# Kernel tuning notes

Measured on AMD Instinct MI355X. Metric: run time of the kernel, lower is better.

Reference implementation:

```python
import jax, jax.numpy as jnp
import numpy as np

HEADS = 8  # diffusers default for hidden_size=320 (head_dim=40)


def setup_inputs() -> dict:
    key = jax.random.key(0)
    k0, k1, k2, k3, k4 = jax.random.split(key, 5)
    batches_of_frames, n, S, C = 1, 5, 1024, 320
    to_k_other = 2
    hidden_states = jax.random.normal(k0, (batches_of_frames * n, S, C), jnp.float32)
    Wq = jax.random.normal(k1, (C, C), jnp.float32) * 0.02
    Wk = jax.random.normal(k2, (C, C), jnp.float32) * 0.02
    Wv = jax.random.normal(k3, (C, C), jnp.float32) * 0.02
    Wo = jax.random.normal(k4, (C, C), jnp.float32) * 0.02
    bo = jnp.zeros((C,), jnp.float32)
    # set_config with random_others=False: self id first, then sequential others
    ids = np.array([[i] + [k for k in range(n) if k != i][:to_k_other] for i in range(n)], dtype=np.int64)
    return {"hidden_states": hidden_states, "Wq": Wq, "Wk": Wk, "Wv": Wv,
            "Wo": Wo, "bo": bo, "ids": jnp.asarray(ids)}


def reference(hidden_states, Wq, Wk, Wv, Wo, bo, ids):
    B, S, C = hidden_states.shape
    n, kf = ids.shape            # frames per group, selected frames per query frame
    Bf = B // n                  # batches_of_frames
    H = HEADS
    d = C // H

    q = hidden_states @ Wq                      # [B, S, C]
    k = hidden_states @ Wk
    v = hidden_states @ Wv

    def gather_frames(x):
        x = x.reshape(Bf, n, S, C)              # expand_batch
        x = x[:, ids]                           # [Bf, n, kf, S, C] cross-frame gather
        return x.reshape(Bf * n, kf * S, C)     # collapse_batch

    k = gather_frames(k)                        # [B, kf*S, C]
    v = gather_frames(v)

    q = q.reshape(B, S, H, d).transpose(0, 2, 1, 3)          # [B, H, S, d]
    k = k.reshape(B, kf * S, H, d).transpose(0, 2, 1, 3)     # [B, H, kf*S, d]
    v = v.reshape(B, kf * S, H, d).transpose(0, 2, 1, 3)

    scale = 1.0 / jnp.sqrt(jnp.asarray(d, q.dtype))
    scores = jnp.einsum('bhqd,bhkd->bhqk', q, k) * scale     # [B, H, S, kf*S]
    probs = jax.nn.softmax(scores, axis=-1)
    attn_out = jnp.einsum('bhqk,bhkd->bhqd', probs, v)       # [B, H, S, d]

    out = attn_out.transpose(0, 2, 1, 3).reshape(B, S, C)    # merge heads
    out = out @ Wo + bo                                      # to_out[0]; to_out[1] dropout = identity
    return out + hidden_states                               # residual, rescale_output_factor=1
```

## Files before the change

kernel.cpp:

```cpp
#include <hip/hip_runtime.h>
#include <hip/hip_bf16.h>

#define NB 5
#define NS 1024
#define NC 320
#define NH 8
#define ND 40
#define NKF 3
#define NBS (NB*NS)
#define NL (NKF*NS)
#define HP 48
#define QSTR 384
#define KTILE (32*48)
#define VTILE (64*32)

typedef __attribute__((ext_vector_type(4))) float f32x4;
typedef __attribute__((ext_vector_type(16))) float f32x16;
typedef __attribute__((ext_vector_type(8))) short bf16x8;
typedef __attribute__((ext_vector_type(4))) unsigned u32x4;

#define MFMA16(a,b,c) __builtin_amdgcn_mfma_f32_16x16x32_bf16((a),(b),(c),0,0,0)
#define MFMA32(a,b,c) __builtin_amdgcn_mfma_f32_32x32x16_bf16((a),(b),(c),0,0,0)

#define QSCALE2 0.22811012f

__device__ inline float ex2(float x){
  float r;
  asm("v_exp_f32 %0, %1" : "=v"(r) : "v"(x));
  return r;
}

__device__ inline unsigned short f2bf(float f){
  unsigned int u = __builtin_bit_cast(unsigned int, f);
  u += 0x7fffu + ((u >> 16) & 1u);
  return (unsigned short)(u >> 16);
}

__device__ inline unsigned pkbf(float lo, float hi){
  unsigned r;
  asm("v_cvt_pk_bf16_f32 %0, %1, %2" : "=v"(r) : "v"(lo), "v"(hi));
  return r;
}

__global__ __launch_bounds__(256) void k_conv_hs(const float* __restrict__ hs,
                                                 unsigned short* __restrict__ hsb){
  int i = (blockIdx.x * 256 + threadIdx.x) * 4;
  float4 v = *(const float4*)&hs[i];
  ushort4 o;
  o.x = f2bf(v.x); o.y = f2bf(v.y); o.z = f2bf(v.z); o.w = f2bf(v.w);
  *(ushort4*)&hsb[i] = o;
}

__global__ void k_conv_w(const float* __restrict__ wq, const float* __restrict__ wk,
                         const float* __restrict__ wv, const float* __restrict__ wo,
                         unsigned short* __restrict__ wqT, unsigned short* __restrict__ wkT,
                         unsigned short* __restrict__ wvT, unsigned short* __restrict__ woT){
  int k = blockIdx.x * 16 + threadIdx.x;
  int n = blockIdx.y * 16 + threadIdx.y;
  const float* src; unsigned short* dst; float scl = 1.0f;
  switch (blockIdx.z){
    case 0: src = wq; dst = wqT; scl = QSCALE2; break;
    case 1: src = wk; dst = wkT; break;
    case 2: src = wv; dst = wvT; break;
    default: src = wo; dst = woT; break;
  }
  dst[n*NC + k] = f2bf(src[k*NC + n] * scl);
}

__global__ __launch_bounds__(256) void k_zero_qbpad(unsigned short* __restrict__ qbp){
  int t = blockIdx.x * 256 + threadIdx.x;
  int token = t >> 3, hh = t & 7;
  bf16x8 z = {0,0,0,0,0,0,0,0};
  *(bf16x8*)&qbp[token*QSTR + hh*HP + ND] = z;
}

__global__ __launch_bounds__(256) void k_qkv(const unsigned short* __restrict__ hsb,
    const unsigned short* __restrict__ wqT, const unsigned short* __restrict__ wkT,
    const unsigned short* __restrict__ wvT,
    unsigned short* __restrict__ qb, unsigned short* __restrict__ kb,
    unsigned short* __restrict__ vT){
  int wave = threadIdx.x >> 6, lane = threadIdx.x & 63;
  int lane16 = lane & 15, grp = lane >> 4;
  int m0 = blockIdx.x * 64, n0 = blockIdx.y * 64;
  int mat = blockIdx.z;
  const unsigned short* wT = (mat == 0) ? wqT : ((mat == 1) ? wkT : wvT);
  int arow = m0 + wave * 16 + lane16;
  f32x4 acc[4];
  #pragma unroll
  for (int t = 0; t < 4; t++) acc[t] = (f32x4){0.f,0.f,0.f,0.f};
  #pragma unroll
  for (int k0 = 0; k0 < NC; k0 += 32){
    bf16x8 a = *(const bf16x8*)&hsb[arow*NC + k0 + grp*8];
    #pragma unroll
    for (int t = 0; t < 4; t++){
      bf16x8 b = *(const bf16x8*)&wT[(n0 + t*16 + lane16)*NC + k0 + grp*8];
      acc[t] = MFMA16(a, b, acc[t]);
    }
  }
  int crow = m0 + wave * 16 + grp * 4;
  #pragma unroll
  for (int t = 0; t < 4; t++){
    int cc = n0 + t*16 + lane16;
    int hh = cc / ND, dd = cc - hh*ND;
    #pragma unroll
    for (int r = 0; r < 4; r++){
      unsigned short val = f2bf(acc[t][r]);
      int rr = crow + r;
      int tokblk = rr >> 5, tl = rr & 31;
      if (mat == 0)      qb[rr*QSTR + hh*HP + dd] = val;
      else if (mat == 1) kb[(((size_t)tokblk*NH + hh)*32 + tl)*HP + dd] = val;
      else               vT[(((size_t)tokblk*NH + hh)*64 + dd)*32 + tl] = val;
    }
  }
}

__global__ __launch_bounds__(192, 3) void k_attn(const unsigned short* __restrict__ qb,
    const unsigned short* __restrict__ kb, const unsigned short* __restrict__ vT,
    const int* __restrict__ ids, unsigned short* __restrict__ ao){
  __shared__ float ldsO[NKF][32][64];
  __shared__ float ldsM[NKF][32];
  __shared__ float ldsL[NKF][32];
  __shared__ float ldsCF[NKF][32];
  int w = threadIdx.x >> 6, lane = threadIdx.x & 63;
  int l31 = lane & 31, hi = lane >> 5;
  int b = blockIdx.z;
  int h = blockIdx.x & 7;
  int q0 = (blockIdx.x >> 3) * 32;
  int frame = ids[b*NKF + w];

  bf16x8 qf0, qf1, qf2;
  {
    int qoff = (b*NS + q0 + l31) * QSTR + h*HP + hi*8;
    qf0 = *(const bf16x8*)&qb[qoff];
    qf1 = *(const bf16x8*)&qb[qoff + 16];
    qf2 = *(const bf16x8*)&qb[qoff + 32];
  }

  const unsigned short* kbase = kb + ((size_t)(frame*32)*NH + h)*KTILE + l31*HP + hi*8;
  const unsigned short* vbase = vT + ((size_t)(frame*32)*NH + h)*VTILE + l31*32 + hi*8;

  f32x16 o0, o1;
  #pragma unroll
  for (int r = 0; r < 16; r++){ o0[r] = 0.f; o1[r] = 0.f; }
  const f32x16 z16 = o0;
  float m2 = -1e30f, lsum = 0.f;

  #pragma unroll 2
  for (int kvb = 0; kvb < NS/32; kvb++){
    const unsigned short* kp = kbase + (size_t)kvb * (NH*KTILE);
    const unsigned short* vp = vbase + (size_t)kvb * (NH*VTILE);
    bf16x8 k0 = *(const bf16x8*)(kp);
    bf16x8 k1 = *(const bf16x8*)(kp + 16);
    bf16x8 k2 = *(const bf16x8*)(kp + 32);
    bf16x8 v00 = *(const bf16x8*)(vp);
    bf16x8 v01 = *(const bf16x8*)(vp + 16);
    bf16x8 v10 = *(const bf16x8*)(vp + 32*32);
    bf16x8 v11 = *(const bf16x8*)(vp + 32*32 + 16);

    f32x16 s = MFMA32(k0, qf0, z16);
    s = MFMA32(k1, qf1, s);
    s = MFMA32(k2, qf2, s);

    float t0 = fmaxf(fmaxf(s[0], s[1]), s[2]);
    float t1 = fmaxf(fmaxf(s[3], s[4]), s[5]);
    float t2 = fmaxf(fmaxf(s[6], s[7]), s[8]);
    float t3 = fmaxf(fmaxf(s[9], s[10]), s[11]);
    float t4 = fmaxf(fmaxf(s[12], s[13]), s[14]);
    float pmax = fmaxf(fmaxf(fmaxf(t0, t1), fmaxf(t2, t3)), fmaxf(t4, s[15]));
    pmax = fmaxf(pmax, __shfl_xor(pmax, 32));

    if (!__all(pmax - m2 <= 8.0f)){
      float mnew = fmaxf(m2, pmax);
      float cf = ex2(m2 - mnew);
      lsum *= cf;
      if (lane < 32) ldsCF[w][l31] = cf;
      #pragma unroll
      for (int r = 0; r < 16; r++){
        float c = ldsCF[w][(r&3) + 8*(r>>2) + 4*hi];
        o0[r] *= c; o1[r] *= c;
      }
      m2 = mnew;
    }

    float p[16];
    #pragma unroll
    for (int r = 0; r < 16; r++) p[r] = ex2(s[r] - m2);
    float a0 = (p[0]+p[1]) + (p[2]+p[3]);
    float a1 = (p[4]+p[5]) + (p[6]+p[7]);
    float a2 = (p[8]+p[9]) + (p[10]+p[11]);
    float a3 = (p[12]+p[13]) + (p[14]+p[15]);
    float ts = (a0+a1) + (a2+a3);
    ts += __shfl_xor(ts, 32);
    lsum += ts;

    u32x4 pw0, pw1;
    #pragma unroll
    for (int ks = 0; ks < 2; ks++){
      int qa = 2*ks + hi;
      int qp = 2*ks + 1 - hi;
      unsigned A0 = pkbf(p[4*qa+0], p[4*qa+1]);
      unsigned A1 = pkbf(p[4*qa+2], p[4*qa+3]);
      unsigned B0 = pkbf(p[4*qp+0], p[4*qp+1]);
      unsigned B1 = pkbf(p[4*qp+2], p[4*qp+3]);
      unsigned R0 = (unsigned)__shfl_xor((int)B0, 32);
      unsigned R1 = (unsigned)__shfl_xor((int)B1, 32);
      u32x4 wd;
      if (hi == 0){ wd[0]=A0; wd[1]=A1; wd[2]=R0; wd[3]=R1; }
      else        { wd[0]=R0; wd[1]=R1; wd[2]=A0; wd[3]=A1; }
      if (ks == 0) pw0 = wd; else pw1 = wd;
    }
    bf16x8 pa0 = __builtin_bit_cast(bf16x8, pw0);
    bf16x8 pa1 = __builtin_bit_cast(bf16x8, pw1);

    o0 = MFMA32(pa0, v00, o0);
    o0 = MFMA32(pa1, v01, o0);
    o1 = MFMA32(pa0, v10, o1);
    o1 = MFMA32(pa1, v11, o1);
  }

  #pragma unroll
  for (int r = 0; r < 16; r++){
    int qq = (r&3) + 8*(r>>2) + 4*hi;
    ldsO[w][qq][l31]      = o0[r];
    ldsO[w][qq][32 + l31] = o1[r];
  }
  if (lane < 32){ ldsM[w][l31] = m2; ldsL[w][l31] = lsum; }
  __syncthreads();

  for (int t = threadIdx.x; t < 32*ND; t += 192){
    int qq = t / ND, d = t - (t / ND) * ND;
    float mA = ldsM[0][qq], mB = ldsM[1][qq], mC = ldsM[2][qq];
    float M = fmaxf(fmaxf(mA, mB), mC);
    float eA = ex2(mA - M), eB = ex2(mB - M), eC = ex2(mC - M);
    float L = ldsL[0][qq]*eA + ldsL[1][qq]*eB + ldsL[2][qq]*eC;
    float O = ldsO[0][qq][d]*eA + ldsO[1][qq][d]*eB + ldsO[2][qq][d]*eC;
    ao[(size_t)(b*NS + q0 + qq)*NC + h*ND + d] = f2bf(O / L);
  }
}

__global__ __launch_bounds__(256) void k_out(const unsigned short* __restrict__ ao,
    const unsigned short* __restrict__ woT, const float* __restrict__ bo,
    const float* __restrict__ hs, float* __restrict__ out){
  int wave = threadIdx.x >> 6, lane = threadIdx.x & 63;
  int lane16 = lane & 15, grp = lane >> 4;
  int m0 = blockIdx.x * 64, n0 = blockIdx.y * 64;
  int arow = m0 + wave*16 + lane16;
  f32x4 acc[4];
  #pragma unroll
  for (int t = 0; t < 4; t++) acc[t] = (f32x4){0.f,0.f,0.f,0.f};
  #pragma unroll
  for (int k0 = 0; k0 < NC; k0 += 32){
    bf16x8 a = *(const bf16x8*)&ao[arow*NC + k0 + grp*8];
    #pragma unroll
    for (int t = 0; t < 4; t++){
      bf16x8 b = *(const bf16x8*)&woT[(n0 + t*16 + lane16)*NC + k0 + grp*8];
      acc[t] = MFMA16(a, b, acc[t]);
    }
  }
  int crow = m0 + wave*16 + grp*4;
  #pragma unroll
  for (int t = 0; t < 4; t++){
    int cc = n0 + t*16 + lane16;
    #pragma unroll
    for (int r = 0; r < 4; r++){
      int rr = crow + r;
      out[rr*NC + cc] = acc[t][r] + bo[cc] + hs[rr*NC + cc];
    }
  }
}

extern "C" void kernel_launch(void* const* d_in, const int* in_sizes, int n_in,
                              void* d_out, int out_size, void* d_ws, size_t ws_size,
                              hipStream_t stream){
  const float* hs = (const float*)d_in[0];
  const float* Wq = (const float*)d_in[1];
  const float* Wk = (const float*)d_in[2];
  const float* Wv = (const float*)d_in[3];
  const float* Wo = (const float*)d_in[4];
  const float* bo = (const float*)d_in[5];
  const int*  ids = (const int*)d_in[6];
  float* out = (float*)d_out;

  unsigned short* hsb = (unsigned short*)d_ws;
  unsigned short* wqT = hsb + (size_t)NBS*NC;
  unsigned short* wkT = wqT + (size_t)NC*NC;
  unsigned short* wvT = wkT + (size_t)NC*NC;
  unsigned short* woT = wvT + (size_t)NC*NC;
  unsigned short* qb  = woT + (size_t)NC*NC;
  unsigned short* kb  = qb  + (size_t)NBS*QSTR;
  unsigned short* vT  = kb  + (size_t)(NBS/32)*NH*KTILE;
  unsigned short* ao  = hsb;

  k_conv_hs<<<dim3(NBS*NC/1024), dim3(256), 0, stream>>>(hs, hsb);
  k_conv_w<<<dim3(NC/16, NC/16, 4), dim3(16,16), 0, stream>>>(Wq, Wk, Wv, Wo, wqT, wkT, wvT, woT);
  k_zero_qbpad<<<dim3(NBS*NH/256), dim3(256), 0, stream>>>(qb);
  k_qkv<<<dim3(NBS/64, NC/64, 3), dim3(256), 0, stream>>>(hsb, wqT, wkT, wvT, qb, kb, vT);
  k_attn<<<dim3((NS/32)*NH, 1, NB), dim3(192), 0, stream>>>(qb, kb, vT, ids, ao);
  k_out<<<dim3(NBS/64, NC/64, 1), dim3(256), 0, stream>>>(ao, woT, bo, hs, out);
}
```

Measured before the change: 280.1 us.

## Double-buffer K/V tile loads with inline asm global loads and vmcnt waits

Replaces the compiler-scheduled per-iteration K/V loads in the attention inner loop with a manual two-stage software pipeline. It issues raw global_load_dwordx4 via inline asm for the next tile while computing the current one, and uses s_waitcnt vmcnt(7) plus sched barriers to wait only for the older batch. The aim is to hide global memory latency behind the QK/PV MFMA and softmax work. The cost is more live registers for two buffers, one redundant clamped load on the last iteration, and fragile asm whose vmcnt accounting must match exactly.

```diff
diff --git a/kernel.cpp b/kernel.cpp
--- a/kernel.cpp
+++ b/kernel.cpp
@@ -23,6 +23,9 @@
 #define MFMA32(a,b,c) __builtin_amdgcn_mfma_f32_32x32x16_bf16((a),(b),(c),0,0,0)
 
 #define QSCALE2 0.22811012f
+
+#define GLOAD(dst, ptr) asm volatile("global_load_dwordx4 %0, %1, off" : "=v"(dst) : "v"(ptr))
+#define WAIT7() do{ asm volatile("s_waitcnt vmcnt(7)" ::: "memory"); __builtin_amdgcn_sched_barrier(0); }while(0)
 
 __device__ inline float ex2(float x){
   float r;
@@ -138,6 +141,7 @@
 
   const unsigned short* kbase = kb + ((size_t)(frame*32)*NH + h)*KTILE + l31*HP + hi*8;
   const unsigned short* vbase = vT + ((size_t)(frame*32)*NH + h)*VTILE + l31*32 + hi*8;
+  const size_t KSTEP = (size_t)NH*KTILE, VSTEP = (size_t)NH*VTILE;
 
   f32x16 o0, o1;
   #pragma unroll
@@ -145,18 +149,8 @@
   const f32x16 z16 = o0;
   float m2 = -1e30f, lsum = 0.f;
 
-  #pragma unroll 2
-  for (int kvb = 0; kvb < NS/32; kvb++){
-    const unsigned short* kp = kbase + (size_t)kvb * (NH*KTILE);
-    const unsigned short* vp = vbase + (size_t)kvb * (NH*VTILE);
-    bf16x8 k0 = *(const bf16x8*)(kp);
-    bf16x8 k1 = *(const bf16x8*)(kp + 16);
-    bf16x8 k2 = *(const bf16x8*)(kp + 32);
-    bf16x8 v00 = *(const bf16x8*)(vp);
-    bf16x8 v01 = *(const bf16x8*)(vp + 16);
-    bf16x8 v10 = *(const bf16x8*)(vp + 32*32);
-    bf16x8 v11 = *(const bf16x8*)(vp + 32*32 + 16);
-
+  auto body = [&](bf16x8 k0, bf16x8 k1, bf16x8 k2,
+                  bf16x8 v00, bf16x8 v01, bf16x8 v10, bf16x8 v11){
     f32x16 s = MFMA32(k0, qf0, z16);
     s = MFMA32(k1, qf1, s);
     s = MFMA32(k2, qf2, s);
@@ -216,6 +210,30 @@
     o0 = MFMA32(pa1, v01, o0);
     o1 = MFMA32(pa0, v10, o1);
     o1 = MFMA32(pa1, v11, o1);
+  };
+
+  bf16x8 Ak0,Ak1,Ak2,Av0,Av1,Av2,Av3, Bk0,Bk1,Bk2,Bv0,Bv1,Bv2,Bv3;
+  GLOAD(Ak0, kbase); GLOAD(Ak1, kbase+16); GLOAD(Ak2, kbase+32);
+  GLOAD(Av0, vbase); GLOAD(Av1, vbase+16); GLOAD(Av2, vbase+1024); GLOAD(Av3, vbase+1024+16);
+
+  for (int kvb = 0; kvb < NS/32; kvb += 2){
+    {
+      const unsigned short* kp = kbase + (size_t)(kvb+1)*KSTEP;
+      const unsigned short* vp = vbase + (size_t)(kvb+1)*VSTEP;
+      GLOAD(Bk0, kp); GLOAD(Bk1, kp+16); GLOAD(Bk2, kp+32);
+      GLOAD(Bv0, vp); GLOAD(Bv1, vp+16); GLOAD(Bv2, vp+1024); GLOAD(Bv3, vp+1024+16);
+    }
+    WAIT7();
+    body(Ak0,Ak1,Ak2,Av0,Av1,Av2,Av3);
+    {
+      int nx = kvb + 2; if (nx > NS/32 - 1) nx = NS/32 - 1;
+      const unsigned short* kp = kbase + (size_t)nx*KSTEP;
+      const unsigned short* vp = vbase + (size_t)nx*VSTEP;
+      GLOAD(Ak0, kp); GLOAD(Ak1, kp+16); GLOAD(Ak2, kp+32);
+      GLOAD(Av0, vp); GLOAD(Av1, vp+16); GLOAD(Av2, vp+1024); GLOAD(Av3, vp+1024+16);
+    }
+    WAIT7();
+    body(Bk0,Bk1,Bk2,Bv0,Bv1,Bv2,Bv3);
   }
 
   #pragma unroll
```

After: 242.0 us. -13.6%, faster.

## Stage K/V tiles into LDS via async global_load_lds with double buffering

Applied to the files above, without the earlier changes.

The attention kernel now copies each 32-token K and V tile into shared memory using direct global-to-LDS loads, double-buffered so the next tile's fetch overlaps the current tile's MFMA work. The QKV projection writes K and V in a new padded 2048-element tile layout with XOR swizzling so the LDS reads avoid bank conflicts. Staging buffers share memory with the final reduction arrays through a union, and occupancy hints drop from 3 to 2 blocks per CU. This trades direct strided global loads for LDS traffic and a manual vmcnt wait, at the risk of lower occupancy and relying on hand-counted wait values.

```diff
diff --git a/kernel.cpp b/kernel.cpp
--- a/kernel.cpp
+++ b/kernel.cpp
@@ -11,8 +11,7 @@
 #define NL (NKF*NS)
 #define HP 48
 #define QSTR 384
-#define KTILE (32*48)
-#define VTILE (64*32)
+#define TSH 2048
 
 typedef __attribute__((ext_vector_type(4))) float f32x4;
 typedef __attribute__((ext_vector_type(16))) float f32x16;
@@ -40,6 +39,13 @@
   unsigned r;
   asm("v_cvt_pk_bf16_f32 %0, %1, %2" : "=v"(r) : "v"(lo), "v"(hi));
   return r;
+}
+
+__device__ inline void stage16(const unsigned short* g, const unsigned short* l){
+  __builtin_amdgcn_global_load_lds(
+    (const __attribute__((address_space(1))) unsigned int*)(g),
+    (__attribute__((address_space(3))) unsigned int*)(l),
+    16, 0, 0);
 }
 
 __global__ __launch_bounds__(256) void k_conv_hs(const float* __restrict__ hs,
@@ -107,20 +113,23 @@
       unsigned short val = f2bf(acc[t][r]);
       int rr = crow + r;
       int tokblk = rr >> 5, tl = rr & 31;
+      size_t tb = ((size_t)tokblk*NH + hh) << 11;
       if (mat == 0)      qb[rr*QSTR + hh*HP + dd] = val;
-      else if (mat == 1) kb[(((size_t)tokblk*NH + hh)*32 + tl)*HP + dd] = val;
-      else               vT[(((size_t)tokblk*NH + hh)*64 + dd)*32 + tl] = val;
-    }
-  }
-}
-
-__global__ __launch_bounds__(192, 3) void k_attn(const unsigned short* __restrict__ qb,
+      else if (mat == 1) kb[tb + tl*64 + (((dd>>3) ^ (tl&7)) << 3) + (dd&7)] = val;
+      else               vT[tb + dd*32 + (((tl>>3) ^ (dd&3)) << 3) + (tl&7)] = val;
+    }
+  }
+}
+
+__global__ __launch_bounds__(192, 2) void k_attn(const unsigned short* __restrict__ qb,
     const unsigned short* __restrict__ kb, const unsigned short* __restrict__ vT,
     const int* __restrict__ ids, unsigned short* __restrict__ ao){
-  __shared__ float ldsO[NKF][32][64];
-  __shared__ float ldsM[NKF][32];
-  __shared__ float ldsL[NKF][32];
+  __shared__ union {
+    unsigned short stg[NKF][2][3584];
+    struct { float O[NKF][32][64]; float M[NKF][32]; float L[NKF][32]; } m;
+  } sh;
   __shared__ float ldsCF[NKF][32];
+
   int w = threadIdx.x >> 6, lane = threadIdx.x & 63;
   int l31 = lane & 31, hi = lane >> 5;
   int b = blockIdx.z;
@@ -136,26 +145,30 @@
     qf2 = *(const bf16x8*)&qb[qoff + 32];
   }
 
-  const unsigned short* kbase = kb + ((size_t)(frame*32)*NH + h)*KTILE + l31*HP + hi*8;
-  const unsigned short* vbase = vT + ((size_t)(frame*32)*NH + h)*VTILE + l31*32 + hi*8;
-
   f32x16 o0, o1;
   #pragma unroll
   for (int r = 0; r < 16; r++){ o0[r] = 0.f; o1[r] = 0.f; }
   const f32x16 z16 = o0;
   float m2 = -1e30f, lsum = 0.f;
 
-  #pragma unroll 2
-  for (int kvb = 0; kvb < NS/32; kvb++){
-    const unsigned short* kp = kbase + (size_t)kvb * (NH*KTILE);
-    const unsigned short* vp = vbase + (size_t)kvb * (NH*VTILE);
-    bf16x8 k0 = *(const bf16x8*)(kp);
-    bf16x8 k1 = *(const bf16x8*)(kp + 16);
-    bf16x8 k2 = *(const bf16x8*)(kp + 32);
-    bf16x8 v00 = *(const bf16x8*)(vp);
-    bf16x8 v01 = *(const bf16x8*)(vp + 16);
-    bf16x8 v10 = *(const bf16x8*)(vp + 32*32);
-    bf16x8 v11 = *(const bf16x8*)(vp + 32*32 + 16);
+  auto stage = [&](int t, int bufi){
+    size_t tb = ((size_t)(frame*32 + t)*NH + h) << 11;
+    const unsigned short* gk = kb + tb;
+    const unsigned short* gv = vT + tb;
+    const unsigned short* sk = &sh.stg[w][bufi][0];
+    const unsigned short* sv = &sh.stg[w][bufi][2048];
+    #pragma unroll
+    for (int i = 0; i < 4; i++) stage16(gk + i*512 + lane*8, sk + i*512);
+    #pragma unroll
+    for (int i = 0; i < 3; i++) stage16(gv + i*512 + lane*8, sv + i*512);
+  };
+
+  auto body = [&](int bufi){
+    const unsigned short* kl = &sh.stg[w][bufi][0];
+    const unsigned short* vl = &sh.stg[w][bufi][2048];
+    bf16x8 k0 = *(const bf16x8*)&kl[l31*64 + (((  hi) ^ (l31&7)) << 3)];
+    bf16x8 k1 = *(const bf16x8*)&kl[l31*64 + (((2+hi) ^ (l31&7)) << 3)];
+    bf16x8 k2 = *(const bf16x8*)&kl[l31*64 + (((4+hi) ^ (l31&7)) << 3)];
 
     f32x16 s = MFMA32(k0, qf0, z16);
     s = MFMA32(k1, qf1, s);
@@ -212,28 +225,47 @@
     bf16x8 pa0 = __builtin_bit_cast(bf16x8, pw0);
     bf16x8 pa1 = __builtin_bit_cast(bf16x8, pw1);
 
+    bf16x8 v00 = *(const bf16x8*)&vl[ l31      *32 + (((  hi) ^ (l31&3)) << 3)];
+    bf16x8 v01 = *(const bf16x8*)&vl[ l31      *32 + (((2+hi) ^ (l31&3)) << 3)];
+    bf16x8 v10 = *(const bf16x8*)&vl[(32+l31)*32 + (((  hi) ^ (l31&3)) << 3)];
+    bf16x8 v11 = *(const bf16x8*)&vl[(32+l31)*32 + (((2+hi) ^ (l31&3)) << 3)];
+
     o0 = MFMA32(pa0, v00, o0);
     o0 = MFMA32(pa1, v01, o0);
     o1 = MFMA32(pa0, v10, o1);
     o1 = MFMA32(pa1, v11, o1);
-  }
-
+  };
+
+  stage(0, 0);
+  int cur = 0;
+  for (int t = 0; t < NS/32 - 1; ++t){
+    stage(t + 1, cur ^ 1);
+    asm volatile("s_waitcnt vmcnt(7)" ::: "memory");
+    __builtin_amdgcn_sched_barrier(0);
+    body(cur);
+    cur ^= 1;
+  }
+  asm volatile("s_waitcnt vmcnt(0)" ::: "memory");
+  __builtin_amdgcn_sched_barrier(0);
+  body(cur);
+
+  __syncthreads();
   #pragma unroll
   for (int r = 0; r < 16; r++){
     int qq = (r&3) + 8*(r>>2) + 4*hi;
-    ldsO[w][qq][l31]      = o0[r];
-    ldsO[w][qq][32 + l31] = o1[r];
-  }
-  if (lane < 32){ ldsM[w][l31] = m2; ldsL[w][l31] = lsum; }
+    sh.m.O[w][qq][l31]      = o0[r];
+    sh.m.O[w][qq][32 + l31] = o1[r];
+  }
+  if (lane < 32){ sh.m.M[w][l31] = m2; sh.m.L[w][l31] = lsum; }
   __syncthreads();
 
   for (int t = threadIdx.x; t < 32*ND; t += 192){
     int qq = t / ND, d = t - (t / ND) * ND;
-    float mA = ldsM[0][qq], mB = ldsM[1][qq], mC = ldsM[2][qq];
+    float mA = sh.m.M[0][qq], mB = sh.m.M[1][qq], mC = sh.m.M[2][qq];
     float M = fmaxf(fmaxf(mA, mB), mC);
     float eA = ex2(mA - M), eB = ex2(mB - M), eC = ex2(mC - M);
-    float L = ldsL[0][qq]*eA + ldsL[1][qq]*eB + ldsL[2][qq]*eC;
-    float O = ldsO[0][qq][d]*eA + ldsO[1][qq][d]*eB + ldsO[2][qq][d]*eC;
+    float L = sh.m.L[0][qq]*eA + sh.m.L[1][qq]*eB + sh.m.L[2][qq]*eC;
+    float O = sh.m.O[0][qq][d]*eA + sh.m.O[1][qq][d]*eB + sh.m.O[2][qq][d]*eC;
     ao[(size_t)(b*NS + q0 + qq)*NC + h*ND + d] = f2bf(O / L);
   }
 }
@@ -288,7 +320,7 @@
   unsigned short* woT = wvT + (size_t)NC*NC;
   unsigned short* qb  = woT + (size_t)NC*NC;
   unsigned short* kb  = qb  + (size_t)NBS*QSTR;
-  unsigned short* vT  = kb  + (size_t)(NBS/32)*NH*KTILE;
+  unsigned short* vT  = kb  + (size_t)(NBS/32)*NH*TSH;
   unsigned short* ao  = hsb;
 
   k_conv_hs<<<dim3(NBS*NC/1024), dim3(256), 0, stream>>>(hs, hsb);
```

After: 241.8 us. 1.16x faster.

## Split attention KV range across six waves and swizzle K/V tile layout

Applied to the files above, without the earlier changes.

Each attention block now runs six waves instead of three, with every frame's 1024-key range split between two waves, and the per-wave partial softmax states are merged in LDS. The K and V tile layouts are padded to 2048 elements and XOR-swizzled so the per-lane 16-byte loads spread across channels and banks. The weight transpose kernel now goes through a shared-memory tile so both its reads and writes are coalesced. The aim is more parallelism per block and shorter serial loops, at the cost of doubled LDS partial storage and a longer merge step.

```diff
diff --git a/kernel.cpp b/kernel.cpp
--- a/kernel.cpp
+++ b/kernel.cpp
@@ -7,12 +7,11 @@
 #define NH 8
 #define ND 40
 #define NKF 3
+#define NSPL 6
 #define NBS (NB*NS)
-#define NL (NKF*NS)
 #define HP 48
 #define QSTR 384
-#define KTILE (32*48)
-#define VTILE (64*32)
+#define TSH 2048
 
 typedef __attribute__((ext_vector_type(4))) float f32x4;
 typedef __attribute__((ext_vector_type(16))) float f32x16;
@@ -55,8 +54,8 @@
                          const float* __restrict__ wv, const float* __restrict__ wo,
                          unsigned short* __restrict__ wqT, unsigned short* __restrict__ wkT,
                          unsigned short* __restrict__ wvT, unsigned short* __restrict__ woT){
-  int k = blockIdx.x * 16 + threadIdx.x;
-  int n = blockIdx.y * 16 + threadIdx.y;
+  __shared__ float tile[16][17];
+  int tx = threadIdx.x, ty = threadIdx.y;
   const float* src; unsigned short* dst; float scl = 1.0f;
   switch (blockIdx.z){
     case 0: src = wq; dst = wqT; scl = QSCALE2; break;
@@ -64,7 +63,9 @@
     case 2: src = wv; dst = wvT; break;
     default: src = wo; dst = woT; break;
   }
-  dst[n*NC + k] = f2bf(src[k*NC + n] * scl);
+  tile[ty][tx] = src[(blockIdx.x*16 + ty)*NC + blockIdx.y*16 + tx];
+  __syncthreads();
+  dst[(blockIdx.y*16 + ty)*NC + blockIdx.x*16 + tx] = f2bf(tile[tx][ty] * scl);
 }
 
 __global__ __launch_bounds__(256) void k_zero_qbpad(unsigned short* __restrict__ qbp){
@@ -107,26 +108,28 @@
       unsigned short val = f2bf(acc[t][r]);
       int rr = crow + r;
       int tokblk = rr >> 5, tl = rr & 31;
+      size_t tb = ((size_t)tokblk*NH + hh) << 11;
       if (mat == 0)      qb[rr*QSTR + hh*HP + dd] = val;
-      else if (mat == 1) kb[(((size_t)tokblk*NH + hh)*32 + tl)*HP + dd] = val;
-      else               vT[(((size_t)tokblk*NH + hh)*64 + dd)*32 + tl] = val;
-    }
-  }
-}
-
-__global__ __launch_bounds__(192, 3) void k_attn(const unsigned short* __restrict__ qb,
+      else if (mat == 1) kb[tb + tl*64 + (((dd>>3) ^ (tl&7)) << 3) + (dd&7)] = val;
+      else               vT[tb + dd*32 + (((tl>>3) ^ (dd&3)) << 3) + (tl&7)] = val;
+    }
+  }
+}
+
+__global__ __launch_bounds__(384) void k_attn(const unsigned short* __restrict__ qb,
     const unsigned short* __restrict__ kb, const unsigned short* __restrict__ vT,
     const int* __restrict__ ids, unsigned short* __restrict__ ao){
-  __shared__ float ldsO[NKF][32][64];
-  __shared__ float ldsM[NKF][32];
-  __shared__ float ldsL[NKF][32];
-  __shared__ float ldsCF[NKF][32];
+  __shared__ float ldsO[NSPL][32][64];
+  __shared__ float ldsM[NSPL][32];
+  __shared__ float ldsL[NSPL][32];
+  __shared__ float ldsCF[NSPL][32];
   int w = threadIdx.x >> 6, lane = threadIdx.x & 63;
   int l31 = lane & 31, hi = lane >> 5;
   int b = blockIdx.z;
   int h = blockIdx.x & 7;
   int q0 = (blockIdx.x >> 3) * 32;
-  int frame = ids[b*NKF + w];
+  int frame = ids[b*NKF + (w >> 1)];
+  int tile0 = (w & 1) * 16;
 
   bf16x8 qf0, qf1, qf2;
   {
@@ -136,8 +139,13 @@
     qf2 = *(const bf16x8*)&qb[qoff + 32];
   }
 
-  const unsigned short* kbase = kb + ((size_t)(frame*32)*NH + h)*KTILE + l31*HP + hi*8;
-  const unsigned short* vbase = vT + ((size_t)(frame*32)*NH + h)*VTILE + l31*32 + hi*8;
+  const int ko0 = l31*64 + (((  hi) ^ (l31&7)) << 3);
+  const int ko1 = l31*64 + (((2+hi) ^ (l31&7)) << 3);
+  const int ko2 = l31*64 + (((4+hi) ^ (l31&7)) << 3);
+  const int vo0 =  l31     *32 + (((  hi) ^ (l31&3)) << 3);
+  const int vo1 =  l31     *32 + (((2+hi) ^ (l31&3)) << 3);
+  const int vo2 = (32+l31)*32 + (((  hi) ^ (l31&3)) << 3);
+  const int vo3 = (32+l31)*32 + (((2+hi) ^ (l31&3)) << 3);
 
   f32x16 o0, o1;
   #pragma unroll
@@ -146,16 +154,17 @@
   float m2 = -1e30f, lsum = 0.f;
 
   #pragma unroll 2
-  for (int kvb = 0; kvb < NS/32; kvb++){
-    const unsigned short* kp = kbase + (size_t)kvb * (NH*KTILE);
-    const unsigned short* vp = vbase + (size_t)kvb * (NH*VTILE);
-    bf16x8 k0 = *(const bf16x8*)(kp);
-    bf16x8 k1 = *(const bf16x8*)(kp + 16);
-    bf16x8 k2 = *(const bf16x8*)(kp + 32);
-    bf16x8 v00 = *(const bf16x8*)(vp);
-    bf16x8 v01 = *(const bf16x8*)(vp + 16);
-    bf16x8 v10 = *(const bf16x8*)(vp + 32*32);
-    bf16x8 v11 = *(const bf16x8*)(vp + 32*32 + 16);
+  for (int i = 0; i < 16; ++i){
+    size_t tb = ((size_t)(frame*32 + tile0 + i)*NH + h) << 11;
+    const unsigned short* kp = kb + tb;
+    const unsigned short* vp = vT + tb;
+    bf16x8 k0 = *(const bf16x8*)(kp + ko0);
+    bf16x8 k1 = *(const bf16x8*)(kp + ko1);
+    bf16x8 k2 = *(const bf16x8*)(kp + ko2);
+    bf16x8 v00 = *(const bf16x8*)(vp + vo0);
+    bf16x8 v01 = *(const bf16x8*)(vp + vo1);
+    bf16x8 v10 = *(const bf16x8*)(vp + vo2);
+    bf16x8 v11 = *(const bf16x8*)(vp + vo3);
 
     f32x16 s = MFMA32(k0, qf0, z16);
     s = MFMA32(k1, qf1, s);
@@ -227,13 +236,18 @@
   if (lane < 32){ ldsM[w][l31] = m2; ldsL[w][l31] = lsum; }
   __syncthreads();
 
-  for (int t = threadIdx.x; t < 32*ND; t += 192){
+  for (int t = threadIdx.x; t < 32*ND; t += 384){
     int qq = t / ND, d = t - (t / ND) * ND;
-    float mA = ldsM[0][qq], mB = ldsM[1][qq], mC = ldsM[2][qq];
-    float M = fmaxf(fmaxf(mA, mB), mC);
-    float eA = ex2(mA - M), eB = ex2(mB - M), eC = ex2(mC - M);
-    float L = ldsL[0][qq]*eA + ldsL[1][qq]*eB + ldsL[2][qq]*eC;
-    float O = ldsO[0][qq][d]*eA + ldsO[1][qq][d]*eB + ldsO[2][qq][d]*eC;
+    float M = -1e30f;
+    #pragma unroll
+    for (int f = 0; f < NSPL; f++) M = fmaxf(M, ldsM[f][qq]);
+    float L = 0.f, O = 0.f;
+    #pragma unroll
+    for (int f = 0; f < NSPL; f++){
+      float e = ex2(ldsM[f][qq] - M);
+      L += ldsL[f][qq]*e;
+      O += ldsO[f][qq][d]*e;
+    }
     ao[(size_t)(b*NS + q0 + qq)*NC + h*ND + d] = f2bf(O / L);
   }
 }
@@ -288,13 +302,13 @@
   unsigned short* woT = wvT + (size_t)NC*NC;
   unsigned short* qb  = woT + (size_t)NC*NC;
   unsigned short* kb  = qb  + (size_t)NBS*QSTR;
-  unsigned short* vT  = kb  + (size_t)(NBS/32)*NH*KTILE;
+  unsigned short* vT  = kb  + (size_t)(NBS/32)*NH*TSH;
   unsigned short* ao  = hsb;
 
   k_conv_hs<<<dim3(NBS*NC/1024), dim3(256), 0, stream>>>(hs, hsb);
   k_conv_w<<<dim3(NC/16, NC/16, 4), dim3(16,16), 0, stream>>>(Wq, Wk, Wv, Wo, wqT, wkT, wvT, woT);
   k_zero_qbpad<<<dim3(NBS*NH/256), dim3(256), 0, stream>>>(qb);
   k_qkv<<<dim3(NBS/64, NC/64, 3), dim3(256), 0, stream>>>(hsb, wqT, wkT, wvT, qb, kb, vT);
-  k_attn<<<dim3((NS/32)*NH, 1, NB), dim3(192), 0, stream>>>(qb, kb, vT, ids, ao);
+  k_attn<<<dim3((NS/32)*NH, 1, NB), dim3(384), 0, stream>>>(qb, kb, vT, ids, ao);
   k_out<<<dim3(NBS/64, NC/64, 1), dim3(256), 0, stream>>>(ao, woT, bo, hs, out);
 }
```

Result: slower. 321.6 us (+14.8%).
